# Performance work log

Measured on AMD Instinct MI355X. Metric: run time of the kernel, lower is better.

The kernel has to match this reference:

```python
import jax, jax.numpy as jnp
import numpy as np

N, E, D, H, G, C = 50000, 600000, 128, 128, 512, 1000
HP = H // 5  # attention-MLP bottleneck (hidden_dim // 5)


def setup_inputs() -> dict:
    key = jax.random.key(0)
    ks = jax.random.split(key, 18)
    cfg_nodes = jax.random.normal(ks[0], (N, D), jnp.float32)
    cfg_relations = jax.random.randint(ks[1], (2, E), 0, N, dtype=jnp.int32)
    pos = jnp.sort(jax.random.randint(ks[2], (G + 1,), 0, N, dtype=jnp.int32))
    node_pos = pos.at[0].set(0).at[-1].set(N)

    def lin(k, fi, fo):
        return jax.random.normal(k, (fi, fo), jnp.float32) / np.sqrt(fi)

    return dict(
        cfg_nodes=cfg_nodes, cfg_relations=cfg_relations, node_pos=node_pos,
        # GATConv layer 1 (in=D, out=H, heads=1)
        W_g1=lin(ks[3], D, H),
        att_src1=jax.random.normal(ks[4], (H,), jnp.float32) / np.sqrt(H),
        att_dst1=jax.random.normal(ks[5], (H,), jnp.float32) / np.sqrt(H),
        b_g1=jnp.zeros((H,), jnp.float32),
        # GATConv layer 2 (in=H, out=H, heads=1, concat=False)
        W_g2=lin(ks[6], H, H),
        att_src2=jax.random.normal(ks[7], (H,), jnp.float32) / np.sqrt(H),
        att_dst2=jax.random.normal(ks[8], (H,), jnp.float32) / np.sqrt(H),
        b_g2=jnp.zeros((H,), jnp.float32),
        # GraphLocalAttention projection MLP
        Wp1=lin(ks[9], H, HP), bp1=jnp.zeros((HP,), jnp.float32),
        Wp2=jax.random.normal(ks[10], (HP,), jnp.float32) / np.sqrt(HP),
        bp2=jnp.zeros((), jnp.float32),
        # final classifier
        Wl=lin(ks[11], H, C), bl=jnp.zeros((C,), jnp.float32),
    )


def _gat_conv(x, src, dst, W, a_src, a_dst, b, n_nodes):
    # PyG GATConv (heads=1): h = xW; e_ij = LeakyReLU(a_s.h_j + a_d.h_i);
    # alpha = softmax over incoming edges of each target; out_i = sum alpha*h_j + b
    h = x @ W                                    # [N, F]
    as_ = h @ a_src                              # [N]
    ad_ = h @ a_dst                              # [N]
    e = jax.nn.leaky_relu(as_[src] + ad_[dst], 0.2)   # [E]
    m = jax.ops.segment_max(e, dst, num_segments=n_nodes)
    ex = jnp.exp(e - m[dst])
    s = jax.ops.segment_sum(ex, dst, num_segments=n_nodes)
    alpha = ex / s[dst]
    out = jax.ops.segment_sum(alpha[:, None] * h[src], dst, num_segments=n_nodes)
    return out + b


def reference(cfg_nodes, cfg_relations, node_pos,
              W_g1, att_src1, att_dst1, b_g1,
              W_g2, att_src2, att_dst2, b_g2,
              Wp1, bp1, Wp2, bp2, Wl, bl):
    n = cfg_nodes.shape[0]
    # add self-loops (PyG GATConv default)
    loops = jnp.arange(n, dtype=cfg_relations.dtype)
    src = jnp.concatenate([cfg_relations[0], loops])
    dst = jnp.concatenate([cfg_relations[1], loops])
    # dropout layers are identity in eval mode
    x = _gat_conv(cfg_nodes, src, dst, W_g1, att_src1, att_dst1, b_g1, n)
    x = jax.nn.elu(x)
    x = _gat_conv(x, src, dst, W_g2, att_src2, att_dst2, b_g2, n)
    # ragged segment attention pooling (attn_by_batch, fully vectorized)
    energy = jax.nn.relu(x @ Wp1 + bp1) @ Wp2 + bp2          # [N]
    seg = jnp.clip(jnp.searchsorted(node_pos, jnp.arange(n), side='right') - 1, 0, G - 1)
    m = jax.ops.segment_max(energy, seg, num_segments=G)
    ex = jnp.exp(energy - m[seg])
    s = jax.ops.segment_sum(ex, seg, num_segments=G)
    w = ex / s[seg]                                           # per-segment softmax
    pooled = jax.ops.segment_sum(w[:, None] * x, seg, num_segments=G)  # [G, H]
    return pooled @ Wl + bl                                   # [G, C]
```

## Files before the change

kernel.cpp:

```cpp
#include <hip/hip_runtime.h>
#include <hip/hip_bf16.h>
#include <math.h>

#define WAVE 64
#define GR 32

typedef __attribute__((ext_vector_type(8))) _Float16 half8;
typedef __attribute__((ext_vector_type(4))) float f32x4;
typedef __attribute__((ext_vector_type(4))) _Float16 half4;

__global__ void count_pack(const int* __restrict__ dst, int* __restrict__ deg, int E, int nbC,
                           const float* __restrict__ W1, const float* __restrict__ W2,
                           _Float16* __restrict__ W1h, _Float16* __restrict__ W2h,
                           const float* __restrict__ Wp1, int HP,
                           _Float16* __restrict__ Ph) {
    int b = blockIdx.x;
    if (b < nbC) {
        int e = (b * 256 + threadIdx.x) * 2;
        if (e + 1 < E) {
            int2 d = *(const int2*)(dst + e);
            atomicAdd(&deg[d.x], 1);
            atomicAdd(&deg[d.y], 1);
        } else if (e < E) {
            atomicAdd(&deg[dst[e]], 1);
        }
    } else if (b < nbC + 128) {
        int pb = b - nbC;
        const float* W = (pb >= 64) ? W2 : W1;
        _Float16* Hf = (pb >= 64) ? W2h : W1h;
        int idx = (pb & 63) * 256 + threadIdx.x;
        int j = idx & 7;
        int lane = (idx >> 3) & 63;
        int kc = (idx >> 9) & 3;
        int nt = idx >> 11;
        int k = kc * 32 + (lane >> 4) * 8 + j;
        int ncol = nt * 16 + (lane & 15);
        Hf[idx] = (_Float16)W[k * 128 + ncol];
    } else {
        int idx = (b - nbC - 128) * 256 + threadIdx.x;
        int j = idx & 7;
        int lane = (idx >> 3) & 63;
        int kc = (idx >> 9) & 3;
        int nt = idx >> 11;
        int k = kc * 32 + (lane >> 4) * 8 + j;
        int ncol = nt * 16 + (lane & 15);
        float x = (ncol < HP) ? Wp1[k * HP + ncol] : 0.f;
        Ph[idx] = (_Float16)x;
    }
}

__global__ void pack_wl(const float* __restrict__ Wl, int C, _Float16* __restrict__ Wlh) {
    int idx = blockIdx.x * 256 + threadIdx.x;
    int j = idx & 7;
    int lane = (idx >> 3) & 63;
    int kc = (idx >> 9) & 3;
    int nt = idx >> 11;
    int k = kc * 32 + (lane >> 4) * 8 + j;
    int ncol = nt * 16 + (lane & 15);
    float x = (ncol < C) ? Wl[(size_t)k * C + ncol] : 0.f;
    Wlh[idx] = (_Float16)x;
}

__global__ void scan_block(const int* __restrict__ in, int* __restrict__ part,
                           int* __restrict__ bsums, int n) {
    __shared__ int tmp[256];
    int tid = threadIdx.x;
    int i = blockIdx.x * 256 + tid;
    int v = (i < n) ? in[i] : 0;
    tmp[tid] = v;
    __syncthreads();
    for (int o = 1; o < 256; o <<= 1) {
        int t = (tid >= o) ? tmp[tid - o] : 0;
        __syncthreads();
        tmp[tid] += t;
        __syncthreads();
    }
    if (i < n) part[i] = tmp[tid] - v;
    if (tid == 255) bsums[blockIdx.x] = tmp[255];
}

__global__ void scan_finish(const int* __restrict__ part, const int* __restrict__ bsums,
                            int* __restrict__ offs, int* __restrict__ cursor,
                            int n, int Etot) {
    __shared__ int acc[256];
    int b = blockIdx.x, tid = threadIdx.x;
    int s = 0;
    for (int i = tid; i < b; i += 256) s += bsums[i];
    acc[tid] = s;
    __syncthreads();
    for (int o = 128; o > 0; o >>= 1) {
        if (tid < o) acc[tid] += acc[tid + o];
        __syncthreads();
    }
    int prefix = acc[0];
    int i = b * 256 + tid;
    if (i < n) {
        int v = part[i] + prefix;
        offs[i] = v;
        cursor[i] = v;
    }
    if (b == 0 && tid == 0) offs[n] = Etot;
}

__global__ void scatter_edges(const int* __restrict__ src, const int* __restrict__ dst,
                              int* __restrict__ cursor, int* __restrict__ csr_src,
                              int* __restrict__ csr_dst, int E) {
    int e = (blockIdx.x * 256 + threadIdx.x) * 2;
    if (e + 1 < E) {
        int2 d = *(const int2*)(dst + e);
        int2 s = *(const int2*)(src + e);
        int p0 = atomicAdd(&cursor[d.x], 1);
        csr_src[p0] = s.x;
        csr_dst[p0] = d.x;
        int p1 = atomicAdd(&cursor[d.y], 1);
        csr_src[p1] = s.y;
        csr_dst[p1] = d.y;
    } else if (e < E) {
        int p = atomicAdd(&cursor[dst[e]], 1);
        csr_src[p] = src[e];
        csr_dst[p] = dst[e];
    }
}

__global__ __launch_bounds__(256) void gemm_mfma(const float* __restrict__ X,
                                                 const _Float16* __restrict__ Bh,
                                                 const float* __restrict__ a_s,
                                                 const float* __restrict__ a_d,
                                                 _Float16* __restrict__ Hout,
                                                 float* __restrict__ as_,
                                                 float* __restrict__ ad_, int n) {
    __shared__ char lds[GR * 136 * 4];
    _Float16* Xh = (_Float16*)lds;
    float* Hs = (float*)lds;

    int tid = threadIdx.x;
    int base = blockIdx.x * GR;
    const float4* X4 = (const float4*)X;

#pragma unroll
    for (int i = 0; i < 4; ++i) {
        int idx = i * 256 + tid;
        int row = idx >> 5, c4 = idx & 31;
        int rs = base + row; if (rs >= n) rs = n - 1;
        float4 v = X4[(size_t)rs * 32 + c4];
        half4 hv = {(_Float16)v.x, (_Float16)v.y, (_Float16)v.z, (_Float16)v.w};
        *(half4*)(Xh + row * 136 + c4 * 4) = hv;
    }
    __syncthreads();

    int wid = tid >> 6, lane = tid & 63;
    int quad = lane >> 4, l16 = lane & 15;
    int rowA = (wid & 1) * 16 + l16;
    int ntb = (wid >> 1) * 4;

    f32x4 acc[4];
#pragma unroll
    for (int t = 0; t < 4; ++t) acc[t] = (f32x4){0.f, 0.f, 0.f, 0.f};

    for (int kc = 0; kc < 4; ++kc) {
        half8 Ah = *(const half8*)(Xh + rowA * 136 + kc * 32 + quad * 8);
#pragma unroll
        for (int nt = 0; nt < 4; ++nt) {
            half8 Bv = *(const half8*)(Bh + (((size_t)((ntb + nt) * 4 + kc)) * 64 + lane) * 8);
            acc[nt] = __builtin_amdgcn_mfma_f32_16x16x32_f16(Ah, Bv, acc[nt], 0, 0, 0);
        }
    }
    __syncthreads();

    int rowD0 = (wid & 1) * 16 + quad * 4;
#pragma unroll
    for (int nt = 0; nt < 4; ++nt)
#pragma unroll
        for (int r = 0; r < 4; ++r)
            Hs[(rowD0 + r) * 136 + (ntb + nt) * 16 + l16] = acc[nt][r];
    __syncthreads();

    const float4* Hs4 = (const float4*)Hs;
    half4* H4 = (half4*)Hout;
#pragma unroll
    for (int i = 0; i < 4; ++i) {
        int idx = i * 256 + tid;
        int row = idx >> 5, c4 = idx & 31;
        int grow = base + row;
        if (grow < n) {
            float4 v = Hs4[row * 34 + c4];
            half4 hv = {(_Float16)v.x, (_Float16)v.y, (_Float16)v.z, (_Float16)v.w};
            H4[(size_t)grow * 32 + c4] = hv;
        }
    }

    int drow = tid >> 3, q = tid & 7;
    const float4* as4 = (const float4*)a_s;
    const float4* ad4 = (const float4*)a_d;
    float s = 0.f, d = 0.f;
#pragma unroll
    for (int j = 0; j < 4; ++j) {
        float4 v = Hs4[drow * 34 + q * 4 + j];
        float4 a = as4[q * 4 + j];
        float4 b = ad4[q * 4 + j];
        s += v.x * a.x + v.y * a.y + v.z * a.z + v.w * a.w;
        d += v.x * b.x + v.y * b.y + v.z * b.z + v.w * b.w;
    }
    s += __shfl_xor(s, 1, WAVE); s += __shfl_xor(s, 2, WAVE); s += __shfl_xor(s, 4, WAVE);
    d += __shfl_xor(d, 1, WAVE); d += __shfl_xor(d, 2, WAVE); d += __shfl_xor(d, 4, WAVE);
    if (q == 0 && base + drow < n) {
        as_[base + drow] = s;
        ad_[base + drow] = d;
    }
}

__global__ __launch_bounds__(256) void gemm_mfma_h(const _Float16* __restrict__ X,
                                                   const _Float16* __restrict__ Bh,
                                                   const float* __restrict__ a_s,
                                                   const float* __restrict__ a_d,
                                                   _Float16* __restrict__ Hout,
                                                   float* __restrict__ as_,
                                                   float* __restrict__ ad_, int n) {
    __shared__ char lds[GR * 136 * 4];
    _Float16* Xh = (_Float16*)lds;
    float* Hs = (float*)lds;

    int tid = threadIdx.x;
    int base = blockIdx.x * GR;
    const half8* X8 = (const half8*)X;

#pragma unroll
    for (int i = 0; i < 2; ++i) {
        int idx = i * 256 + tid;
        int row = idx >> 4, c8 = idx & 15;
        int rs = base + row; if (rs >= n) rs = n - 1;
        *(half8*)(Xh + row * 136 + c8 * 8) = X8[(size_t)rs * 16 + c8];
    }
    __syncthreads();

    int wid = tid >> 6, lane = tid & 63;
    int quad = lane >> 4, l16 = lane & 15;
    int rowA = (wid & 1) * 16 + l16;
    int ntb = (wid >> 1) * 4;

    f32x4 acc[4];
#pragma unroll
    for (int t = 0; t < 4; ++t) acc[t] = (f32x4){0.f, 0.f, 0.f, 0.f};

    for (int kc = 0; kc < 4; ++kc) {
        half8 Ah = *(const half8*)(Xh + rowA * 136 + kc * 32 + quad * 8);
#pragma unroll
        for (int nt = 0; nt < 4; ++nt) {
            half8 Bv = *(const half8*)(Bh + (((size_t)((ntb + nt) * 4 + kc)) * 64 + lane) * 8);
            acc[nt] = __builtin_amdgcn_mfma_f32_16x16x32_f16(Ah, Bv, acc[nt], 0, 0, 0);
        }
    }
    __syncthreads();

    int rowD0 = (wid & 1) * 16 + quad * 4;
#pragma unroll
    for (int nt = 0; nt < 4; ++nt)
#pragma unroll
        for (int r = 0; r < 4; ++r)
            Hs[(rowD0 + r) * 136 + (ntb + nt) * 16 + l16] = acc[nt][r];
    __syncthreads();

    const float4* Hs4 = (const float4*)Hs;
    half4* H4 = (half4*)Hout;
#pragma unroll
    for (int i = 0; i < 4; ++i) {
        int idx = i * 256 + tid;
        int row = idx >> 5, c4 = idx & 31;
        int grow = base + row;
        if (grow < n) {
            float4 v = Hs4[row * 34 + c4];
            half4 hv = {(_Float16)v.x, (_Float16)v.y, (_Float16)v.z, (_Float16)v.w};
            H4[(size_t)grow * 32 + c4] = hv;
        }
    }

    int drow = tid >> 3, q = tid & 7;
    const float4* as4 = (const float4*)a_s;
    const float4* ad4 = (const float4*)a_d;
    float s = 0.f, d = 0.f;
#pragma unroll
    for (int j = 0; j < 4; ++j) {
        float4 v = Hs4[drow * 34 + q * 4 + j];
        float4 a = as4[q * 4 + j];
        float4 b = ad4[q * 4 + j];
        s += v.x * a.x + v.y * a.y + v.z * a.z + v.w * a.w;
        d += v.x * b.x + v.y * b.y + v.z * b.z + v.w * b.w;
    }
    s += __shfl_xor(s, 1, WAVE); s += __shfl_xor(s, 2, WAVE); s += __shfl_xor(s, 4, WAVE);
    d += __shfl_xor(d, 1, WAVE); d += __shfl_xor(d, 2, WAVE); d += __shfl_xor(d, 4, WAVE);
    if (q == 0 && base + drow < n) {
        as_[base + drow] = s;
        ad_[base + drow] = d;
    }
}

__device__ __forceinline__ float leaky02(float x) { return x > 0.f ? x : 0.2f * x; }

__global__ __launch_bounds__(256) void edge_weights(const int* __restrict__ csr_src,
                                                    const int* __restrict__ csr_dst,
                                                    const float* __restrict__ as_,
                                                    const float* __restrict__ ad_,
                                                    int2* __restrict__ sw, int E) {
    int i = (blockIdx.x * 256 + threadIdx.x) * 4;
    if (i + 3 < E) {
        int4 s = *(const int4*)(csr_src + i);
        int4 d = *(const int4*)(csr_dst + i);
        float wx = __expf(leaky02(as_[s.x] + ad_[d.x]));
        float wy = __expf(leaky02(as_[s.y] + ad_[d.y]));
        float wz = __expf(leaky02(as_[s.z] + ad_[d.z]));
        float ww = __expf(leaky02(as_[s.w] + ad_[d.w]));
        int4 lo = make_int4(s.x, __float_as_int(wx), s.y, __float_as_int(wy));
        int4 hi = make_int4(s.z, __float_as_int(wz), s.w, __float_as_int(ww));
        *(int4*)(sw + i) = lo;
        *(int4*)(sw + i + 2) = hi;
    } else {
        for (; i < E; ++i) {
            float w = __expf(leaky02(as_[csr_src[i]] + ad_[csr_dst[i]]));
            sw[i] = make_int2(csr_src[i], __float_as_int(w));
        }
    }
}

__global__ __launch_bounds__(256) void gat_aggregate(const _Float16* __restrict__ h,
                                                     const int2* __restrict__ sw,
                                                     const float* __restrict__ as_,
                                                     const float* __restrict__ ad_,
                                                     const int* __restrict__ offs,
                                                     const float* __restrict__ bias,
                                                     _Float16* __restrict__ out, int n, int act) {
    int node = blockIdx.x * 4 + (threadIdx.x >> 6);
    int lane = threadIdx.x & 63;
    if (node >= n) return;
    int beg = offs[node], end = offs[node + 1];
    int q4 = lane >> 4, l = lane & 15;
    const half8* h8 = (const half8*)h;

    float w_self = __expf(leaky02(as_[node] + ad_[node]));
    float facc[8];
    {
        half8 v = h8[(size_t)node * 16 + l];
        float ws = (q4 == 0) ? w_self : 0.f;
#pragma unroll
        for (int i = 0; i < 8; ++i) facc[i] = ws * (float)v[i];
    }
    float sacc = (lane == 0) ? w_self : 0.f;
#pragma unroll 2
    for (int j = beg; j < end; j += 4) {
        int j0 = j + q4;
        bool valid = j0 < end;
        int jc = valid ? j0 : (end - 1);
        int2 e = sw[jc];
        int s = valid ? e.x : node;
        float w = valid ? __int_as_float(e.y) : 0.f;
        half8 v = h8[(size_t)s * 16 + l];
#pragma unroll
        for (int i = 0; i < 8; ++i) facc[i] = fmaf(w, (float)v[i], facc[i]);
        sacc += (l == 0) ? w : 0.f;
    }
#pragma unroll
    for (int i = 0; i < 8; ++i) {
        facc[i] += __shfl_xor(facc[i], 16, WAVE);
        facc[i] += __shfl_xor(facc[i], 32, WAVE);
    }
    sacc += __shfl_xor(sacc, 16, WAVE);
    sacc += __shfl_xor(sacc, 32, WAVE);
    float inv_s = 1.f / __shfl(sacc, 0, WAVE);
    if (q4 == 0) {
        const float4* b4 = (const float4*)bias;
        float4 b0 = b4[l * 2], b1 = b4[l * 2 + 1];
        float o[8];
        o[0] = fmaf(facc[0], inv_s, b0.x);
        o[1] = fmaf(facc[1], inv_s, b0.y);
        o[2] = fmaf(facc[2], inv_s, b0.z);
        o[3] = fmaf(facc[3], inv_s, b0.w);
        o[4] = fmaf(facc[4], inv_s, b1.x);
        o[5] = fmaf(facc[5], inv_s, b1.y);
        o[6] = fmaf(facc[6], inv_s, b1.z);
        o[7] = fmaf(facc[7], inv_s, b1.w);
        if (act == 1) {
#pragma unroll
            for (int i = 0; i < 8; ++i) o[i] = o[i] > 0.f ? o[i] : expm1f(o[i]);
        }
        half8 hv;
#pragma unroll
        for (int i = 0; i < 8; ++i) hv[i] = (_Float16)o[i];
        ((half8*)(out + (size_t)node * 128))[l] = hv;
    }
}

__global__ __launch_bounds__(256) void energy_mfma(const _Float16* __restrict__ X,
                                                   const _Float16* __restrict__ Ph,
                                                   const float* __restrict__ bp1,
                                                   const float* __restrict__ Wp2,
                                                   const float* __restrict__ bp2,
                                                   float* __restrict__ energy, int n, int HP) {
    __shared__ _Float16 Xh[GR * 136];
    int tid = threadIdx.x;
    int base = blockIdx.x * GR;
    const half8* X8 = (const half8*)X;
#pragma unroll
    for (int i = 0; i < 2; ++i) {
        int idx = i * 256 + tid;
        int row = idx >> 4, c8 = idx & 15;
        int rs = base + row; if (rs >= n) rs = n - 1;
        *(half8*)(Xh + row * 136 + c8 * 8) = X8[(size_t)rs * 16 + c8];
    }
    __syncthreads();

    int wid = tid >> 6, lane = tid & 63;
    if (wid >= 2) return;
    int quad = lane >> 4, l16 = lane & 15;
    int rowA = wid * 16 + l16;

    f32x4 acc0 = (f32x4){0.f, 0.f, 0.f, 0.f};
    f32x4 acc1 = (f32x4){0.f, 0.f, 0.f, 0.f};
    for (int kc = 0; kc < 4; ++kc) {
        half8 Ah = *(const half8*)(Xh + rowA * 136 + kc * 32 + quad * 8);
        half8 B0 = *(const half8*)(Ph + (((size_t)kc) * 64 + lane) * 8);
        half8 B1 = *(const half8*)(Ph + (((size_t)(4 + kc)) * 64 + lane) * 8);
        acc0 = __builtin_amdgcn_mfma_f32_16x16x32_f16(Ah, B0, acc0, 0, 0, 0);
        acc1 = __builtin_amdgcn_mfma_f32_16x16x32_f16(Ah, B1, acc1, 0, 0, 0);
    }

    float b0 = bp1[l16];
    float w0 = Wp2[l16];
    int c1 = 16 + l16;
    int c1c = c1 < HP ? c1 : HP - 1;
    float b1 = bp1[c1c];
    float w1 = (c1 < HP) ? Wp2[c1c] : 0.f;
    float bp2v = bp2[0];
#pragma unroll
    for (int r = 0; r < 4; ++r) {
        float h0 = acc0[r] + b0;
        h0 = h0 > 0.f ? h0 : 0.f;
        float h1 = acc1[r] + b1;
        h1 = h1 > 0.f ? h1 : 0.f;
        float v = h0 * w0 + h1 * w1;
        v += __shfl_xor(v, 1, WAVE);
        v += __shfl_xor(v, 2, WAVE);
        v += __shfl_xor(v, 4, WAVE);
        v += __shfl_xor(v, 8, WAVE);
        int row = base + wid * 16 + quad * 4 + r;
        if (l16 == 0 && row < n) energy[row] = v + bp2v;
    }
}

__global__ __launch_bounds__(256) void seg_pool(const _Float16* __restrict__ X,
                                                const float* __restrict__ energy,
                                                const int* __restrict__ node_pos,
                                                float* __restrict__ pooled) {
    int g = blockIdx.x >> 1;
    int bn = blockIdx.x & 1;
    int beg = node_pos[g], end = node_pos[g + 1];
    int tid = threadIdx.x;
    int wid = tid >> 6, lane = tid & 63;
    __shared__ float swr[8];
    __shared__ float4 red[256];

    float m = -INFINITY;
    for (int i = beg + tid; i < end; i += 256) m = fmaxf(m, energy[i]);
#pragma unroll
    for (int o = 1; o < 64; o <<= 1) m = fmaxf(m, __shfl_xor(m, o, WAVE));
    if (lane == 0) swr[wid] = m;
    __syncthreads();
    m = fmaxf(fmaxf(swr[0], swr[1]), fmaxf(swr[2], swr[3]));

    float s = 0.f;
    for (int i = beg + tid; i < end; i += 256) s += __expf(energy[i] - m);
#pragma unroll
    for (int o = 1; o < 64; o <<= 1) s += __shfl_xor(s, o, WAVE);
    if (lane == 0) swr[4 + wid] = s;
    __syncthreads();
    s = swr[4] + swr[5] + swr[6] + swr[7];
    float inv = (end > beg && s > 0.f) ? 1.f / s : 0.f;

    int cq = tid & 15;
    int rg = tid >> 4;
    const half4* X4 = (const half4*)X;
    float4 acc = make_float4(0.f, 0.f, 0.f, 0.f);
#pragma unroll 2
    for (int i = beg + rg; i < end; i += 16) {
        float w = __expf(energy[i] - m) * inv;
        half4 v = X4[(size_t)i * 32 + bn * 16 + cq];
        acc.x = fmaf(w, (float)v.x, acc.x);
        acc.y = fmaf(w, (float)v.y, acc.y);
        acc.z = fmaf(w, (float)v.z, acc.z);
        acc.w = fmaf(w, (float)v.w, acc.w);
    }
    red[tid] = acc;
#pragma unroll
    for (int o = 8; o >= 1; o >>= 1) {
        __syncthreads();
        if (rg < o) {
            float4 t = red[tid + o * 16];
            acc.x += t.x; acc.y += t.y; acc.z += t.z; acc.w += t.w;
            red[tid] = acc;
        }
    }
    if (rg == 0)
        ((float4*)(pooled + (size_t)g * 128 + bn * 64))[cq] = acc;
}

__global__ __launch_bounds__(256) void classify_mfma(const float* __restrict__ P,
                                                     const _Float16* __restrict__ Wlh,
                                                     const float* __restrict__ bl,
                                                     float* __restrict__ out,
                                                     int G_, int C, int nbM) {
    __shared__ _Float16 Xh[GR * 136];
    int tid = threadIdx.x;
    int bm = blockIdx.x % nbM;
    int bn = blockIdx.x / nbM;
    int base = bm * GR;
    const float4* X4 = (const float4*)P;
#pragma unroll
    for (int i = 0; i < 4; ++i) {
        int idx = i * 256 + tid;
        int row = idx >> 5, c4 = idx & 31;
        int rs = base + row; if (rs >= G_) rs = G_ - 1;
        float4 v = X4[(size_t)rs * 32 + c4];
        half4 hv = {(_Float16)v.x, (_Float16)v.y, (_Float16)v.z, (_Float16)v.w};
        *(half4*)(Xh + row * 136 + c4 * 4) = hv;
    }
    __syncthreads();

    int wid = tid >> 6, lane = tid & 63;
    int quad = lane >> 4, l16 = lane & 15;
    int rowA = (wid & 1) * 16 + l16;
    int ntb = bn * 8 + (wid >> 1) * 4;

    f32x4 acc[4];
#pragma unroll
    for (int t = 0; t < 4; ++t) acc[t] = (f32x4){0.f, 0.f, 0.f, 0.f};

    for (int kc = 0; kc < 4; ++kc) {
        half8 Ah = *(const half8*)(Xh + rowA * 136 + kc * 32 + quad * 8);
#pragma unroll
        for (int nt = 0; nt < 4; ++nt) {
            half8 Bv = *(const half8*)(Wlh + (((size_t)((ntb + nt) * 4 + kc)) * 64 + lane) * 8);
            acc[nt] = __builtin_amdgcn_mfma_f32_16x16x32_f16(Ah, Bv, acc[nt], 0, 0, 0);
        }
    }

    int row0 = base + (wid & 1) * 16 + quad * 4;
#pragma unroll
    for (int nt = 0; nt < 4; ++nt) {
        int col = (ntb + nt) * 16 + l16;
        if (col < C) {
            float b = bl[col];
#pragma unroll
            for (int r = 0; r < 4; ++r) {
                int row = row0 + r;
                if (row < G_) out[(size_t)row * C + col] = acc[nt][r] + b;
            }
        }
    }
}

extern "C" void kernel_launch(void* const* d_in, const int* in_sizes, int n_in,
                              void* d_out, int out_size, void* d_ws, size_t ws_size,
                              hipStream_t stream) {
    const float* cfg_nodes = (const float*)d_in[0];
    const int* rel = (const int*)d_in[1];
    const int* node_pos = (const int*)d_in[2];
    const float* W_g1 = (const float*)d_in[3];
    const float* att_src1 = (const float*)d_in[4];
    const float* att_dst1 = (const float*)d_in[5];
    const float* b_g1 = (const float*)d_in[6];
    const float* W_g2 = (const float*)d_in[7];
    const float* att_src2 = (const float*)d_in[8];
    const float* att_dst2 = (const float*)d_in[9];
    const float* b_g2 = (const float*)d_in[10];
    const float* Wp1 = (const float*)d_in[11];
    const float* bp1 = (const float*)d_in[12];
    const float* Wp2 = (const float*)d_in[13];
    const float* bp2 = (const float*)d_in[14];
    const float* Wl = (const float*)d_in[15];
    const float* bl = (const float*)d_in[16];

    const int N = in_sizes[0] / 128;
    const int E = in_sizes[1] / 2;
    const int G = in_sizes[2] - 1;
    const int HP = in_sizes[12];
    const int C = out_size / G;

    const int* srcArr = rel;
    const int* dstArr = rel + E;

    char* w = (char*)d_ws;
    auto carve = [&](size_t bytes) -> char* {
        char* p = w;
        w += (bytes + 255) & ~(size_t)255;
        return p;
    };
    _Float16* bufH = (_Float16*)carve((size_t)N * 128 * 2);
    _Float16* bufF = (_Float16*)carve((size_t)N * 128 * 2);
    float* asv = (float*)carve((size_t)N * 4);
    float* adv = (float*)carve((size_t)N * 4);
    float* energy = (float*)carve((size_t)N * 4);
    int* deg = (int*)carve((size_t)N * 4);
    int* offs = (int*)carve((size_t)(N + 1) * 4);
    int* cursor = (int*)carve((size_t)N * 4);
    int* csr_src = (int*)carve((size_t)E * 4);
    int* csr_dst = (int*)carve((size_t)E * 4);
    int2* swbuf = (int2*)carve((size_t)E * 8);
    int* bsums = (int*)carve(1024);
    _Float16* W1h = (_Float16*)carve(16384 * 2);
    _Float16* W2h = (_Float16*)carve(16384 * 2);
    _Float16* Ph = (_Float16*)carve(4096 * 2);
    _Float16* Wlh = (_Float16*)carve(131072 * 2);
    float* pooled = (float*)carve((size_t)G * 128 * 4);

    const int nbN = (N + 255) / 256;
    const int nbC = ((E + 1) / 2 + 255) / 256;
    const int nbT = (N + GR - 1) / GR;
    const int nbW = (E + 1023) / 1024;
    const int nbM = (G + GR - 1) / GR;
    const int nbCt = (C + 127) / 128;

    hipMemsetAsync(deg, 0, (size_t)N * 4, stream);
    count_pack<<<nbC + 144, 256, 0, stream>>>(dstArr, deg, E, nbC,
                                              W_g1, W_g2, W1h, W2h, Wp1, HP, Ph);
    pack_wl<<<512, 256, 0, stream>>>(Wl, C, Wlh);
    scan_block<<<nbN, 256, 0, stream>>>(deg, offs, bsums, N);
    scan_finish<<<nbN, 256, 0, stream>>>(offs, bsums, offs, cursor, N, E);
    scatter_edges<<<nbC, 256, 0, stream>>>(srcArr, dstArr, cursor, csr_src, csr_dst, E);

    gemm_mfma<<<nbT, 256, 0, stream>>>(cfg_nodes, W1h, att_src1, att_dst1,
                                       bufH, asv, adv, N);
    edge_weights<<<nbW, 256, 0, stream>>>(csr_src, csr_dst, asv, adv, swbuf, E);
    gat_aggregate<<<(N + 3) / 4, 256, 0, stream>>>(bufH, swbuf, asv, adv, offs, b_g1, bufF, N, 1);

    gemm_mfma_h<<<nbT, 256, 0, stream>>>(bufF, W2h, att_src2, att_dst2,
                                         bufH, asv, adv, N);
    edge_weights<<<nbW, 256, 0, stream>>>(csr_src, csr_dst, asv, adv, swbuf, E);
    gat_aggregate<<<(N + 3) / 4, 256, 0, stream>>>(bufH, swbuf, asv, adv, offs, b_g2, bufF, N, 0);

    energy_mfma<<<nbT, 256, 0, stream>>>(bufF, Ph, bp1, Wp2, bp2, energy, N, HP);
    seg_pool<<<G * 2, 256, 0, stream>>>(bufF, energy, node_pos, pooled);
    classify_mfma<<<nbM * nbCt, 256, 0, stream>>>(pooled, Wlh, bl, (float*)d_out, G, C, nbM);
}
```

Baseline: 301.1 us.

## Interleave CSR src/dst, double-buffer aggregation loads, use all waves in energy kernel

```diff
diff --git a/kernel.cpp b/kernel.cpp
--- a/kernel.cpp
+++ b/kernel.cpp
@@ -103,22 +103,18 @@
 }
 
 __global__ void scatter_edges(const int* __restrict__ src, const int* __restrict__ dst,
-                              int* __restrict__ cursor, int* __restrict__ csr_src,
-                              int* __restrict__ csr_dst, int E) {
+                              int* __restrict__ cursor, int2* __restrict__ csr_sd, int E) {
     int e = (blockIdx.x * 256 + threadIdx.x) * 2;
     if (e + 1 < E) {
         int2 d = *(const int2*)(dst + e);
         int2 s = *(const int2*)(src + e);
         int p0 = atomicAdd(&cursor[d.x], 1);
-        csr_src[p0] = s.x;
-        csr_dst[p0] = d.x;
+        csr_sd[p0] = make_int2(s.x, d.x);
         int p1 = atomicAdd(&cursor[d.y], 1);
-        csr_src[p1] = s.y;
-        csr_dst[p1] = d.y;
+        csr_sd[p1] = make_int2(s.y, d.y);
     } else if (e < E) {
         int p = atomicAdd(&cursor[dst[e]], 1);
-        csr_src[p] = src[e];
-        csr_dst[p] = dst[e];
+        csr_sd[p] = make_int2(src[e], dst[e]);
     }
 }
 
@@ -296,27 +292,27 @@
 
 __device__ __forceinline__ float leaky02(float x) { return x > 0.f ? x : 0.2f * x; }
 
-__global__ __launch_bounds__(256) void edge_weights(const int* __restrict__ csr_src,
-                                                    const int* __restrict__ csr_dst,
+__global__ __launch_bounds__(256) void edge_weights(const int2* __restrict__ csr_sd,
                                                     const float* __restrict__ as_,
                                                     const float* __restrict__ ad_,
                                                     int2* __restrict__ sw, int E) {
     int i = (blockIdx.x * 256 + threadIdx.x) * 4;
     if (i + 3 < E) {
-        int4 s = *(const int4*)(csr_src + i);
-        int4 d = *(const int4*)(csr_dst + i);
-        float wx = __expf(leaky02(as_[s.x] + ad_[d.x]));
-        float wy = __expf(leaky02(as_[s.y] + ad_[d.y]));
-        float wz = __expf(leaky02(as_[s.z] + ad_[d.z]));
-        float ww = __expf(leaky02(as_[s.w] + ad_[d.w]));
-        int4 lo = make_int4(s.x, __float_as_int(wx), s.y, __float_as_int(wy));
-        int4 hi = make_int4(s.z, __float_as_int(wz), s.w, __float_as_int(ww));
+        int4 p0 = *(const int4*)(csr_sd + i);
+        int4 p1 = *(const int4*)(csr_sd + i + 2);
+        float wx = __expf(leaky02(as_[p0.x] + ad_[p0.y]));
+        float wy = __expf(leaky02(as_[p0.z] + ad_[p0.w]));
+        float wz = __expf(leaky02(as_[p1.x] + ad_[p1.y]));
+        float ww = __expf(leaky02(as_[p1.z] + ad_[p1.w]));
+        int4 lo = make_int4(p0.x, __float_as_int(wx), p0.z, __float_as_int(wy));
+        int4 hi = make_int4(p1.x, __float_as_int(wz), p1.z, __float_as_int(ww));
         *(int4*)(sw + i) = lo;
         *(int4*)(sw + i + 2) = hi;
     } else {
         for (; i < E; ++i) {
-            float w = __expf(leaky02(as_[csr_src[i]] + ad_[csr_dst[i]]));
-            sw[i] = make_int2(csr_src[i], __float_as_int(w));
+            int2 sd = csr_sd[i];
+            float w = __expf(leaky02(as_[sd.x] + ad_[sd.y]));
+            sw[i] = make_int2(sd.x, __float_as_int(w));
         }
     }
 }
@@ -336,29 +332,39 @@
     const half8* h8 = (const half8*)h;
 
     float w_self = __expf(leaky02(as_[node] + ad_[node]));
-    float facc[8];
+    float facc[8], facc2[8];
     {
         half8 v = h8[(size_t)node * 16 + l];
         float ws = (q4 == 0) ? w_self : 0.f;
 #pragma unroll
-        for (int i = 0; i < 8; ++i) facc[i] = ws * (float)v[i];
+        for (int i = 0; i < 8; ++i) { facc[i] = ws * (float)v[i]; facc2[i] = 0.f; }
     }
     float sacc = (lane == 0) ? w_self : 0.f;
-#pragma unroll 2
-    for (int j = beg; j < end; j += 4) {
+    for (int j = beg; j < end; j += 8) {
         int j0 = j + q4;
-        bool valid = j0 < end;
-        int jc = valid ? j0 : (end - 1);
-        int2 e = sw[jc];
-        int s = valid ? e.x : node;
-        float w = valid ? __int_as_float(e.y) : 0.f;
-        half8 v = h8[(size_t)s * 16 + l];
-#pragma unroll
-        for (int i = 0; i < 8; ++i) facc[i] = fmaf(w, (float)v[i], facc[i]);
-        sacc += (l == 0) ? w : 0.f;
+        int j1 = j + 4 + q4;
+        bool vA = j0 < end;
+        bool vB = j1 < end;
+        int jA = vA ? j0 : (end - 1);
+        int jB = vB ? j1 : (end - 1);
+        int2 eA = sw[jA];
+        int2 eB = sw[jB];
+        int sA = vA ? eA.x : node;
+        int sB = vB ? eB.x : node;
+        float wA = vA ? __int_as_float(eA.y) : 0.f;
+        float wB = vB ? __int_as_float(eB.y) : 0.f;
+        half8 a = h8[(size_t)sA * 16 + l];
+        half8 b = h8[(size_t)sB * 16 + l];
+#pragma unroll
+        for (int i = 0; i < 8; ++i) {
+            facc[i]  = fmaf(wA, (float)a[i], facc[i]);
+            facc2[i] = fmaf(wB, (float)b[i], facc2[i]);
+        }
+        sacc += (l == 0) ? (wA + wB) : 0.f;
     }
 #pragma unroll
     for (int i = 0; i < 8; ++i) {
+        facc[i] += facc2[i];
         facc[i] += __shfl_xor(facc[i], 16, WAVE);
         facc[i] += __shfl_xor(facc[i], 32, WAVE);
     }
@@ -388,18 +394,19 @@
     }
 }
 
+#define GR2 64
 __global__ __launch_bounds__(256) void energy_mfma(const _Float16* __restrict__ X,
                                                    const _Float16* __restrict__ Ph,
                                                    const float* __restrict__ bp1,
                                                    const float* __restrict__ Wp2,
                                                    const float* __restrict__ bp2,
                                                    float* __restrict__ energy, int n, int HP) {
-    __shared__ _Float16 Xh[GR * 136];
+    __shared__ _Float16 Xh[GR2 * 136];
     int tid = threadIdx.x;
-    int base = blockIdx.x * GR;
+    int base = blockIdx.x * GR2;
     const half8* X8 = (const half8*)X;
 #pragma unroll
-    for (int i = 0; i < 2; ++i) {
+    for (int i = 0; i < 4; ++i) {
         int idx = i * 256 + tid;
         int row = idx >> 4, c8 = idx & 15;
         int rs = base + row; if (rs >= n) rs = n - 1;
@@ -408,7 +415,6 @@
     __syncthreads();
 
     int wid = tid >> 6, lane = tid & 63;
-    if (wid >= 2) return;
     int quad = lane >> 4, l16 = lane & 15;
     int rowA = wid * 16 + l16;
 
@@ -600,8 +606,7 @@
     int* deg = (int*)carve((size_t)N * 4);
     int* offs = (int*)carve((size_t)(N + 1) * 4);
     int* cursor = (int*)carve((size_t)N * 4);
-    int* csr_src = (int*)carve((size_t)E * 4);
-    int* csr_dst = (int*)carve((size_t)E * 4);
+    int2* csr_sd = (int2*)carve((size_t)E * 8);
     int2* swbuf = (int2*)carve((size_t)E * 8);
     int* bsums = (int*)carve(1024);
     _Float16* W1h = (_Float16*)carve(16384 * 2);
@@ -613,6 +618,7 @@
     const int nbN = (N + 255) / 256;
     const int nbC = ((E + 1) / 2 + 255) / 256;
     const int nbT = (N + GR - 1) / GR;
+    const int nbT2 = (N + GR2 - 1) / GR2;
     const int nbW = (E + 1023) / 1024;
     const int nbM = (G + GR - 1) / GR;
     const int nbCt = (C + 127) / 128;
@@ -623,19 +629,19 @@
     pack_wl<<<512, 256, 0, stream>>>(Wl, C, Wlh);
     scan_block<<<nbN, 256, 0, stream>>>(deg, offs, bsums, N);
     scan_finish<<<nbN, 256, 0, stream>>>(offs, bsums, offs, cursor, N, E);
-    scatter_edges<<<nbC, 256, 0, stream>>>(srcArr, dstArr, cursor, csr_src, csr_dst, E);
+    scatter_edges<<<nbC, 256, 0, stream>>>(srcArr, dstArr, cursor, csr_sd, E);
 
     gemm_mfma<<<nbT, 256, 0, stream>>>(cfg_nodes, W1h, att_src1, att_dst1,
                                        bufH, asv, adv, N);
-    edge_weights<<<nbW, 256, 0, stream>>>(csr_src, csr_dst, asv, adv, swbuf, E);
+    edge_weights<<<nbW, 256, 0, stream>>>(csr_sd, asv, adv, swbuf, E);
     gat_aggregate<<<(N + 3) / 4, 256, 0, stream>>>(bufH, swbuf, asv, adv, offs, b_g1, bufF, N, 1);
 
     gemm_mfma_h<<<nbT, 256, 0, stream>>>(bufF, W2h, att_src2, att_dst2,
                                          bufH, asv, adv, N);
-    edge_weights<<<nbW, 256, 0, stream>>>(csr_src, csr_dst, asv, adv, swbuf, E);
+    edge_weights<<<nbW, 256, 0, stream>>>(csr_sd, asv, adv, swbuf, E);
     gat_aggregate<<<(N + 3) / 4, 256, 0, stream>>>(bufH, swbuf, asv, adv, offs, b_g2, bufF, N, 0);
 
-    energy_mfma<<<nbT, 256, 0, stream>>>(bufF, Ph, bp1, Wp2, bp2, energy, N, HP);
+    energy_mfma<<<nbT2, 256, 0, stream>>>(bufF, Ph, bp1, Wp2, bp2, energy, N, HP);
     seg_pool<<<G * 2, 256, 0, stream>>>(bufF, energy, node_pos, pooled);
     classify_mfma<<<nbM * nbCt, 256, 0, stream>>>(pooled, Wlh, bl, (float*)d_out, G, C, nbM);
 }
```

Measured after the change: 298.6 us. About the same (-0.8%).
